# Optimization experiments

Measured on AMD Instinct MI355X. Metric: run time of the kernel, lower is better.

## Reference

```python
import jax, jax.numpy as jnp
import numpy as np

# --- module hyperparameters (from init_kwargs) ---
FREQUENCY = jnp.array([0.5, 0.3, 0.7, 0.2], dtype=jnp.float32)
SCALE = 1.0
CONCENTRATION = 1.0
THRESHOLD = 0.1
CLIP_MAX = 0.9  # hard-coded 0.9 in the original clip

# --- graph dims ---
N_NODES, D_NODE = 50000, 128
N_EDGES, D_EDGE = 3200000, 16
TIME = 3


def setup_inputs() -> dict:
    key = jax.random.key(0)
    ks = jax.random.split(key, 7)
    nodes = jax.random.normal(ks[0], (N_NODES, D_NODE), jnp.float32)
    edges = jax.random.normal(ks[1], (N_EDGES, D_EDGE), jnp.float32)
    rec = jax.random.randint(ks[2], (N_EDGES,), 0, N_NODES, dtype=jnp.int64)
    send = jax.random.randint(ks[3], (N_EDGES,), 0, N_NODES, dtype=jnp.int64)
    aedges = (jax.random.uniform(ks[4], (N_EDGES,)) < 0.95).astype(jnp.float32)
    u_weibull = jax.random.uniform(ks[5], (1,), jnp.float32)  # drives weibull_min draw
    u_edges = jax.random.uniform(ks[6], (N_EDGES,), jnp.float32)  # per-edge dropout draws
    return {
        "nodes": nodes,
        "edges": edges,
        "aedges": aedges,
        "u_weibull": u_weibull,
        "u_edges": u_edges,
        "rec": rec,
        "send": send,
        "time": TIME,
    }


def reference(nodes, edges, aedges, u_weibull, u_edges, rec, send, time):
    # --- get_ratio: weibull_min sample via inverse CDF, modulating base frequency ---
    base_freq = FREQUENCY[time % FREQUENCY.shape[0]]
    w = SCALE * (-jnp.log1p(-u_weibull[0])) ** (1.0 / CONCENTRATION)
    ratio = jnp.clip(base_freq * w, 0.0, CLIP_MAX)
    ratio = jnp.where(ratio < THRESHOLD, 0.0, ratio)

    # --- _rm_edges: bernoulli dropout + argsort compaction + gathers ---
    degens = (u_edges < ratio).astype(jnp.float32)
    naedges = aedges * (1.0 - degens)          # [E] in {0,1}
    idxs = jnp.argsort(1.0 - naedges)          # active edges first (stable)
    naedges = naedges[idxs]
    active = naedges > 0
    sentinel = nodes.shape[0] - 1
    nrec = jnp.where(active, rec[idxs], sentinel)
    nsend = jnp.where(active, send[idxs], sentinel)
    new_edges = jnp.where(active[:, None], edges[idxs], 0.0)  # [E, D_EDGE]
    return naedges, nrec, nsend, new_edges
```

## Files before the change

kernel.cpp:

```cpp
#include <hip/hip_runtime.h>
#include <hip/hip_bf16.h>
#include <math.h>

#define BLOCK 256
#define ITEMS 4
#define TILE (BLOCK * ITEMS)

typedef float f4v __attribute__((ext_vector_type(4)));

__device__ __forceinline__ float compute_ratio(const float* uw, const int* timep) {
  int t = timep[0];
  t = ((t % 4) + 4) % 4;
  float base = (t == 0) ? 0.5f : (t == 1) ? 0.3f : (t == 2) ? 0.7f : 0.2f;
  double u = (double)uw[0];
  float w = (float)(-log1p(-u));
  float r = base * w;
  r = fminf(fmaxf(r, 0.0f), 0.9f);
  if (r < 0.1f) r = 0.0f;
  return r;
}

__global__ __launch_bounds__(BLOCK, 8) void passA(
    const float* __restrict__ aedges, const float* __restrict__ ue,
    const float* __restrict__ uw, const int* __restrict__ timep,
    const unsigned* __restrict__ rec32, const unsigned* __restrict__ send32,
    unsigned* __restrict__ bsums, unsigned char* __restrict__ masks,
    unsigned* __restrict__ flagp, int use_masks, int E) {
  __shared__ float s_ratio;
  __shared__ unsigned s_w[BLOCK / 64];
  const int tid = threadIdx.x;
  if (tid == 0) s_ratio = compute_ratio(uw, timep);
  if (blockIdx.x == 0 && tid < 64) {
    unsigned acc = 0;
#pragma unroll
    for (int j = 0; j < 4; ++j) {
      const int i = tid + j * 64;
      acc |= rec32[2 * i + 1];
      acc |= send32[2 * i + 1];
    }
#pragma unroll
    for (int d = 1; d < 64; d <<= 1) acc |= __shfl_xor(acc, d);
    if (tid == 0) flagp[0] = (acc == 0u) ? 1u : 0u;
  }
  __syncthreads();
  const float ratio = s_ratio;
  const long long base = (long long)blockIdx.x * TILE + (long long)tid * ITEMS;
  unsigned m = 0;
  if (base + ITEMS <= (long long)E) {
    const f4v a0 = *(const f4v*)(aedges + base);
    const f4v u0 = *(const f4v*)(ue + base);
    const float av[4] = {a0.x, a0.y, a0.z, a0.w};
    const float uv[4] = {u0.x, u0.y, u0.z, u0.w};
#pragma unroll
    for (int j = 0; j < 4; ++j)
      if (av[j] != 0.0f && uv[j] >= ratio) m |= (1u << j);
  } else {
    for (int j = 0; j < 4; ++j) {
      long long i = base + j;
      if (i < (long long)E && aedges[i] != 0.0f && ue[i] >= ratio) m |= (1u << j);
    }
  }
  if (use_masks) masks[(size_t)blockIdx.x * BLOCK + tid] = (unsigned char)m;
  unsigned c = __popc(m);
#pragma unroll
  for (int d = 1; d < 64; d <<= 1) c += __shfl_xor(c, d);
  if ((tid & 63) == 0) s_w[tid >> 6] = c;
  __syncthreads();
  if (tid == 0) bsums[blockIdx.x] = s_w[0] + s_w[1] + s_w[2] + s_w[3];
}

__global__ __launch_bounds__(BLOCK, 8) void passC(
    const float* __restrict__ aedges, const float* __restrict__ ue,
    const float* __restrict__ uw, const int* __restrict__ timep,
    const int* __restrict__ rec32, const int* __restrict__ send32,
    const float* __restrict__ edges,
    const unsigned* __restrict__ bsums, int nblocks,
    const unsigned* __restrict__ flagp,
    const unsigned char* __restrict__ masks, int use_masks,
    float* __restrict__ out, int E, int sentinel) {
  __shared__ float s_ratio;
  __shared__ unsigned s_w[BLOCK / 64];
  __shared__ unsigned s_i64;
  __shared__ unsigned long long s_red[BLOCK / 64];
  __shared__ unsigned short s_sidx[TILE];
  __shared__ unsigned short s_rec[TILE];
  __shared__ unsigned short s_send[TILE];
  const int tid = threadIdx.x;
  const int b = blockIdx.x;
  if (tid == 0) { s_ratio = compute_ratio(uw, timep); s_i64 = flagp[0]; }
  __syncthreads();
  const bool is64 = (s_i64 != 0u);
  const long long tileBase = (long long)b * TILE;
  const int local_n = (int)min((long long)TILE, (long long)E - tileBase);
  const long long base = tileBase + (long long)tid * ITEMS;
  const unsigned short sent16 = (unsigned short)sentinel;

  unsigned m = 0;
  if (use_masks) {
    m = (unsigned)masks[(size_t)b * BLOCK + tid];
  } else {
    const float ratio = s_ratio;
    if (base + ITEMS <= (long long)E) {
      const f4v a0 = *(const f4v*)(aedges + base);
      const f4v u0 = *(const f4v*)(ue + base);
      const float av[4] = {a0.x, a0.y, a0.z, a0.w};
      const float uv[4] = {u0.x, u0.y, u0.z, u0.w};
#pragma unroll
      for (int j = 0; j < 4; ++j)
        if (av[j] != 0.0f && uv[j] >= ratio) m |= (1u << j);
    } else {
      for (int j = 0; j < 4; ++j) {
        long long i = base + j;
        if (i < (long long)E && aedges[i] != 0.0f && ue[i] >= ratio) m |= (1u << j);
      }
    }
  }

  const unsigned c = __popc(m);
  unsigned x = c;
#pragma unroll
  for (int d = 1; d < 64; d <<= 1) {
    unsigned t = __shfl_up(x, d);
    if ((tid & 63) >= d) x += t;
  }
  if ((tid & 63) == 63) s_w[tid >> 6] = x;
  __syncthreads();
  unsigned woff = 0;
  for (int w = 0; w < (tid >> 6); ++w) woff += s_w[w];
  const unsigned cnt = s_w[0] + s_w[1] + s_w[2] + s_w[3];
  const unsigned thread_excl = woff + (x - c);

  const int nk = (nblocks + BLOCK - 1) / BLOCK;
  unsigned long long pr = 0;
  for (int k = 0; k < nk; ++k) {
    const int idx = tid + k * BLOCK;
    const unsigned v = (idx < nblocks) ? bsums[idx] : 0u;
    pr += ((unsigned long long)v << 32);
    if (idx < b) pr += v;
  }
#pragma unroll
  for (int d = 1; d < 64; d <<= 1) pr += __shfl_xor(pr, d);
  if ((tid & 63) == 0) s_red[tid >> 6] = pr;

#pragma unroll
  for (int j = 0; j < ITEMS; ++j) {
    const int li = tid * ITEMS + j;
    if (li >= local_n) break;
    const long long i = base + j;
    const bool act = ((m >> j) & 1u) != 0u;
    const unsigned rb = __popc(m & ((1u << j) - 1u));
    const unsigned actsBefore = thread_excl + rb;
    const unsigned dr = act ? actsBefore : (cnt + ((unsigned)li - actsBefore));
    unsigned short rv = sent16, sv = sent16;
    if (act) {
      if (is64) {
        rv = (unsigned short)((const long long*)rec32)[i];
        sv = (unsigned short)((const long long*)send32)[i];
      } else {
        rv = (unsigned short)rec32[i];
        sv = (unsigned short)send32[i];
      }
    }
    s_sidx[dr] = (unsigned short)li;
    s_rec[dr] = rv;
    s_send[dr] = sv;
  }
  __syncthreads();

  const unsigned long long tt = s_red[0] + s_red[1] + s_red[2] + s_red[3];
  const unsigned gA = (unsigned)(tt & 0xffffffffull);
  const unsigned nA = (unsigned)(tt >> 32);
  const unsigned gI = nA + (unsigned)tileBase - gA;

  float* __restrict__ out_na = out;
  float* __restrict__ out_rec = out + (size_t)E;
  float* __restrict__ out_send = out + 2 * (size_t)E;
  float* __restrict__ out_edges = out + 3 * (size_t)E;
  const f4v zero4 = {0.f, 0.f, 0.f, 0.f};
  const int sub = tid & 3;

  if (local_n == TILE) {
#pragma unroll
    for (int k = 0; k < ITEMS; ++k) {
      const int r = tid + k * BLOCK;
      const bool ra = (unsigned)r < cnt;
      const unsigned dest = ra ? (gA + (unsigned)r) : (gI + ((unsigned)r - cnt));
      __builtin_nontemporal_store(ra ? 1.0f : 0.0f, out_na + dest);
      __builtin_nontemporal_store((float)s_rec[r], out_rec + dest);
      __builtin_nontemporal_store((float)s_send[r], out_send + dest);
    }
#pragma unroll 8
    for (int k = 0; k < TILE / (BLOCK / 4); ++k) {
      const int r = (tid >> 2) + k * (BLOCK / 4);
      const bool ra = (unsigned)r < cnt;
      const unsigned dest = ra ? (gA + (unsigned)r) : (gI + ((unsigned)r - cnt));
      f4v v = zero4;
      if (ra) {
        const int si = (int)s_sidx[r];
        v = ((const f4v*)edges)[(size_t)(tileBase + si) * 4 + sub];
      }
      __builtin_nontemporal_store(v, (f4v*)out_edges + (size_t)dest * 4 + sub);
    }
  } else {
    for (int k = 0; k < ITEMS; ++k) {
      const int r = tid + k * BLOCK;
      if (r >= local_n) break;
      const bool ra = (unsigned)r < cnt;
      const unsigned dest = ra ? (gA + (unsigned)r) : (gI + ((unsigned)r - cnt));
      out_na[dest] = ra ? 1.0f : 0.0f;
      out_rec[dest] = (float)s_rec[r];
      out_send[dest] = (float)s_send[r];
    }
    for (int k = 0; k < TILE / (BLOCK / 4); ++k) {
      const int r = (tid >> 2) + k * (BLOCK / 4);
      if (r >= local_n) break;
      const bool ra = (unsigned)r < cnt;
      const unsigned dest = ra ? (gA + (unsigned)r) : (gI + ((unsigned)r - cnt));
      f4v v = zero4;
      if (ra) {
        const int si = (int)s_sidx[r];
        v = ((const f4v*)edges)[(size_t)(tileBase + si) * 4 + sub];
      }
      ((f4v*)out_edges)[(size_t)dest * 4 + sub] = v;
    }
  }
}

extern "C" void kernel_launch(void* const* d_in, const int* in_sizes, int n_in,
                              void* d_out, int out_size, void* d_ws, size_t ws_size,
                              hipStream_t stream) {
  const float* edges = (const float*)d_in[1];
  const float* aedges = (const float*)d_in[2];
  const float* uw = (const float*)d_in[3];
  const float* ue = (const float*)d_in[4];
  const int* rec = (const int*)d_in[5];
  const int* send = (const int*)d_in[6];
  const int* timep = (const int*)d_in[7];

  const int E = in_sizes[2];
  const int n_nodes = in_sizes[0] / 128;
  const int sentinel = n_nodes - 1;
  const int nblocks = (E + TILE - 1) / TILE;

  unsigned* bsums = (unsigned*)d_ws;
  unsigned* flagp = bsums + (nblocks + 2);
  unsigned char* masks = (unsigned char*)(bsums + nblocks + 16);
  const size_t need = (size_t)(nblocks + 16) * 4 + (size_t)nblocks * BLOCK + 64;
  const int use_masks = (ws_size >= need) ? 1 : 0;
  float* out = (float*)d_out;

  hipLaunchKernelGGL(passA, dim3(nblocks), dim3(BLOCK), 0, stream,
                     aedges, ue, uw, timep, (const unsigned*)rec,
                     (const unsigned*)send, bsums, masks, flagp, use_masks, E);
  hipLaunchKernelGGL(passC, dim3(nblocks), dim3(BLOCK), 0, stream,
                     aedges, ue, uw, timep, rec, send, edges, bsums, nblocks,
                     flagp, masks, use_masks, out, E, sentinel);
}
```

Baseline: 88.84 us.

## Use two-level group sums for block offsets and vectorize index loads

```diff
diff --git a/kernel.cpp b/kernel.cpp
--- a/kernel.cpp
+++ b/kernel.cpp
@@ -5,6 +5,8 @@
 #define BLOCK 256
 #define ITEMS 4
 #define TILE (BLOCK * ITEMS)
+#define GSHIFT 8
+#define MAXGROUPS 256
 
 typedef float f4v __attribute__((ext_vector_type(4)));
 
@@ -24,7 +26,8 @@
     const float* __restrict__ aedges, const float* __restrict__ ue,
     const float* __restrict__ uw, const int* __restrict__ timep,
     const unsigned* __restrict__ rec32, const unsigned* __restrict__ send32,
-    unsigned* __restrict__ bsums, unsigned char* __restrict__ masks,
+    unsigned* __restrict__ bsums, unsigned* __restrict__ gsums,
+    unsigned char* __restrict__ masks,
     unsigned* __restrict__ flagp, int use_masks, int E) {
   __shared__ float s_ratio;
   __shared__ unsigned s_w[BLOCK / 64];
@@ -66,7 +69,11 @@
   for (int d = 1; d < 64; d <<= 1) c += __shfl_xor(c, d);
   if ((tid & 63) == 0) s_w[tid >> 6] = c;
   __syncthreads();
-  if (tid == 0) bsums[blockIdx.x] = s_w[0] + s_w[1] + s_w[2] + s_w[3];
+  if (tid == 0) {
+    const unsigned cnt = s_w[0] + s_w[1] + s_w[2] + s_w[3];
+    bsums[blockIdx.x] = cnt;
+    atomicAdd(&gsums[blockIdx.x >> GSHIFT], cnt);
+  }
 }
 
 __global__ __launch_bounds__(BLOCK, 8) void passC(
@@ -74,14 +81,14 @@
     const float* __restrict__ uw, const int* __restrict__ timep,
     const int* __restrict__ rec32, const int* __restrict__ send32,
     const float* __restrict__ edges,
-    const unsigned* __restrict__ bsums, int nblocks,
-    const unsigned* __restrict__ flagp,
+    const unsigned* __restrict__ bsums, const unsigned* __restrict__ gsums,
+    int nblocks, const unsigned* __restrict__ flagp,
     const unsigned char* __restrict__ masks, int use_masks,
     float* __restrict__ out, int E, int sentinel) {
   __shared__ float s_ratio;
   __shared__ unsigned s_w[BLOCK / 64];
   __shared__ unsigned s_i64;
-  __shared__ unsigned long long s_red[BLOCK / 64];
+  __shared__ unsigned s_red[BLOCK / 64];
   __shared__ unsigned short s_sidx[TILE];
   __shared__ unsigned short s_rec[TILE];
   __shared__ unsigned short s_send[TILE];
@@ -93,14 +100,33 @@
   const long long tileBase = (long long)b * TILE;
   const int local_n = (int)min((long long)TILE, (long long)E - tileBase);
   const long long base = tileBase + (long long)tid * ITEMS;
+  const bool full = (base + ITEMS <= (long long)E);
   const unsigned short sent16 = (unsigned short)sentinel;
+
+  const int ngroups = (nblocks + (1 << GSHIFT) - 1) >> GSHIFT;
+  const int g = b >> GSHIFT;
+  const int gbase = g << GSHIFT;
+  unsigned gpre = 0, gtot = 0;
+  for (int gg = 0; gg < ngroups; ++gg) {
+    const unsigned v = gsums[gg];
+    gtot += v;
+    if (gg < g) gpre += v;
+  }
+  {
+    const int idx = gbase + tid;
+    const unsigned v = (idx < nblocks) ? bsums[idx] : 0u;
+    unsigned wp = (idx < b) ? v : 0u;
+#pragma unroll
+    for (int d = 1; d < 64; d <<= 1) wp += __shfl_xor(wp, d);
+    if ((tid & 63) == 0) s_red[tid >> 6] = wp;
+  }
 
   unsigned m = 0;
   if (use_masks) {
     m = (unsigned)masks[(size_t)b * BLOCK + tid];
   } else {
     const float ratio = s_ratio;
-    if (base + ITEMS <= (long long)E) {
+    if (full) {
       const f4v a0 = *(const f4v*)(aedges + base);
       const f4v u0 = *(const f4v*)(ue + base);
       const float av[4] = {a0.x, a0.y, a0.z, a0.w};
@@ -130,46 +156,58 @@
   const unsigned cnt = s_w[0] + s_w[1] + s_w[2] + s_w[3];
   const unsigned thread_excl = woff + (x - c);
 
-  const int nk = (nblocks + BLOCK - 1) / BLOCK;
-  unsigned long long pr = 0;
-  for (int k = 0; k < nk; ++k) {
-    const int idx = tid + k * BLOCK;
-    const unsigned v = (idx < nblocks) ? bsums[idx] : 0u;
-    pr += ((unsigned long long)v << 32);
-    if (idx < b) pr += v;
-  }
-#pragma unroll
-  for (int d = 1; d < 64; d <<= 1) pr += __shfl_xor(pr, d);
-  if ((tid & 63) == 0) s_red[tid >> 6] = pr;
-
+  unsigned short rvs[ITEMS], svs[ITEMS];
+  if (full && is64) {
+    const long long* rp = (const long long*)rec32 + base;
+    const long long* sp = (const long long*)send32 + base;
+    const ulonglong2 r01 = *(const ulonglong2*)rp;
+    const ulonglong2 r23 = *(const ulonglong2*)(rp + 2);
+    const ulonglong2 t01 = *(const ulonglong2*)sp;
+    const ulonglong2 t23 = *(const ulonglong2*)(sp + 2);
+    rvs[0] = (unsigned short)r01.x; rvs[1] = (unsigned short)r01.y;
+    rvs[2] = (unsigned short)r23.x; rvs[3] = (unsigned short)r23.y;
+    svs[0] = (unsigned short)t01.x; svs[1] = (unsigned short)t01.y;
+    svs[2] = (unsigned short)t23.x; svs[3] = (unsigned short)t23.y;
+  } else if (full) {
+    const uint4 rr = *(const uint4*)((const unsigned*)rec32 + base);
+    const uint4 ss = *(const uint4*)((const unsigned*)send32 + base);
+    rvs[0] = (unsigned short)rr.x; rvs[1] = (unsigned short)rr.y;
+    rvs[2] = (unsigned short)rr.z; rvs[3] = (unsigned short)rr.w;
+    svs[0] = (unsigned short)ss.x; svs[1] = (unsigned short)ss.y;
+    svs[2] = (unsigned short)ss.z; svs[3] = (unsigned short)ss.w;
+  } else {
+#pragma unroll
+    for (int j = 0; j < 4; ++j) {
+      const long long i = base + j;
+      unsigned short rv = sent16, sv = sent16;
+      if (i < (long long)E) {
+        if (is64) {
+          rv = (unsigned short)((const long long*)rec32)[i];
+          sv = (unsigned short)((const long long*)send32)[i];
+        } else {
+          rv = (unsigned short)rec32[i];
+          sv = (unsigned short)send32[i];
+        }
+      }
+      rvs[j] = rv; svs[j] = sv;
+    }
+  }
 #pragma unroll
   for (int j = 0; j < ITEMS; ++j) {
     const int li = tid * ITEMS + j;
     if (li >= local_n) break;
-    const long long i = base + j;
     const bool act = ((m >> j) & 1u) != 0u;
     const unsigned rb = __popc(m & ((1u << j) - 1u));
     const unsigned actsBefore = thread_excl + rb;
     const unsigned dr = act ? actsBefore : (cnt + ((unsigned)li - actsBefore));
-    unsigned short rv = sent16, sv = sent16;
-    if (act) {
-      if (is64) {
-        rv = (unsigned short)((const long long*)rec32)[i];
-        sv = (unsigned short)((const long long*)send32)[i];
-      } else {
-        rv = (unsigned short)rec32[i];
-        sv = (unsigned short)send32[i];
-      }
-    }
     s_sidx[dr] = (unsigned short)li;
-    s_rec[dr] = rv;
-    s_send[dr] = sv;
-  }
-  __syncthreads();
-
-  const unsigned long long tt = s_red[0] + s_red[1] + s_red[2] + s_red[3];
-  const unsigned gA = (unsigned)(tt & 0xffffffffull);
-  const unsigned nA = (unsigned)(tt >> 32);
+    s_rec[dr] = act ? rvs[j] : sent16;
+    s_send[dr] = act ? svs[j] : sent16;
+  }
+  __syncthreads();
+
+  const unsigned gA = gpre + s_red[0] + s_red[1] + s_red[2] + s_red[3];
+  const unsigned nA = gtot;
   const unsigned gI = nA + (unsigned)tileBase - gA;
 
   float* __restrict__ out_na = out;
@@ -243,16 +281,21 @@
   const int nblocks = (E + TILE - 1) / TILE;
 
   unsigned* bsums = (unsigned*)d_ws;
-  unsigned* flagp = bsums + (nblocks + 2);
-  unsigned char* masks = (unsigned char*)(bsums + nblocks + 16);
-  const size_t need = (size_t)(nblocks + 16) * 4 + (size_t)nblocks * BLOCK + 64;
+  unsigned* flagp = bsums + nblocks;
+  unsigned* gsums = bsums + nblocks + 4;
+  unsigned char* masks = (unsigned char*)(gsums + MAXGROUPS + 4);
+  const size_t need = (size_t)(nblocks + MAXGROUPS + 16) * 4 +
+                      (size_t)nblocks * BLOCK + 64;
   const int use_masks = (ws_size >= need) ? 1 : 0;
   float* out = (float*)d_out;
 
+  hipMemsetAsync(gsums, 0, MAXGROUPS * sizeof(unsigned), stream);
+
   hipLaunchKernelGGL(passA, dim3(nblocks), dim3(BLOCK), 0, stream,
                      aedges, ue, uw, timep, (const unsigned*)rec,
-                     (const unsigned*)send, bsums, masks, flagp, use_masks, E);
+                     (const unsigned*)send, bsums, gsums, masks, flagp,
+                     use_masks, E);
   hipLaunchKernelGGL(passC, dim3(nblocks), dim3(BLOCK), 0, stream,
-                     aedges, ue, uw, timep, rec, send, edges, bsums, nblocks,
-                     flagp, masks, use_masks, out, E, sentinel);
+                     aedges, ue, uw, timep, rec, send, edges, bsums, gsums,
+                     nblocks, flagp, masks, use_masks, out, E, sentinel);
 }
```

Result: slower. 115.2 us (+29.7%).
